# Performance work log

Measured on AMD Instinct MI355X. Metric: run time of the kernel, lower is better.

## Reference

```python
import jax, jax.numpy as jnp
import numpy as np

EPS = 1e-12  # torch F.normalize eps
K = 32       # num_clusters (hardcoded in module)

def l2norm(v, axis):
    n = jnp.sqrt(jnp.sum(v * v, axis=axis, keepdims=True))
    return v / jnp.maximum(n, EPS)

def setup_inputs() -> dict:
    key = jax.random.key(0)
    k1, k2, k3, k4 = jax.random.split(key, 4)
    B, M, D = 64, 128, 2048
    x = jax.random.normal(k1, (B, M, D), dtype=jnp.float32)
    # ragged lengths in [1, M]
    lengths = jax.random.randint(k2, (B,), 0, M, dtype=jnp.int32) + 1
    init_sc = 1.0 / np.sqrt(D)
    W = init_sc * jax.random.normal(k3, (K, D), dtype=jnp.float32)  # fc1.weight
    C = init_sc * jax.random.normal(k4, (K, D), dtype=jnp.float32)  # centroids
    return {"x": x, "lengths": lengths, "W": W, "C": C}

def reference(x, lengths, W, C):
    # x: [B,M,D] padded frames, lengths: [B] valid frame counts
    B, M, D = x.shape
    mask = (jnp.arange(M)[None, :] < lengths[:, None]).astype(x.dtype)  # [B,M]
    cnt = lengths.astype(x.dtype)[:, None]                              # [B,1]
    # avg pooling over valid (raw, un-normalized) frames
    avgpool = jnp.sum(x * mask[:, :, None], axis=1) / cnt               # [B,D]
    # per-frame L2 normalize
    xn = l2norm(x, axis=-1)                                             # [B,M,D]
    # soft assignment: linear (no bias) + softmax over clusters
    logits = jnp.einsum('bmd,kd->bmk', xn, W)
    a = jax.nn.softmax(logits, axis=-1) * mask[:, :, None]              # [B,M,K]
    # VLAD residual aggregation, GEMM form:
    # sum_m a[b,m,k]*(xn[b,m,:] - C[k,:]) = (a^T xn) - C * sum_m a
    ax = jnp.einsum('bmk,bmd->bkd', a, xn)                              # [B,K,D]
    asum = jnp.sum(a, axis=1)                                           # [B,K]
    vlad = ax - asum[:, :, None] * C[None, :, :]                        # [B,K,D]
    # intra-normalize per cluster, flatten, global L2 normalize
    vlad = l2norm(vlad, axis=2)
    vlad = vlad.reshape(B, K * D)
    vlad = l2norm(vlad, axis=1)
    return jnp.concatenate([avgpool, vlad], axis=1)                     # [B, D + K*D]
```

## Files before the change

kernel.cpp:

```cpp
#include <hip/hip_runtime.h>
#include <math.h>

#define BB 64
#define MM 128
#define DDIM 2048
#define KK 32
#define NFR (BB*MM)
#define OUTROW (DDIM + KK*DDIM)

typedef __attribute__((ext_vector_type(8))) short bf16x8;
typedef __attribute__((ext_vector_type(4))) float f32x4;

__device__ __forceinline__ short f2bf(float f) {
  unsigned u = __builtin_bit_cast(unsigned, f);
  u += 0x7fffu + ((u >> 16) & 1u);
  return (short)(u >> 16);
}
__device__ __forceinline__ unsigned pack2(float lo, float hi) {
  return (unsigned)(unsigned short)f2bf(lo) | ((unsigned)(unsigned short)f2bf(hi) << 16);
}

__global__ __launch_bounds__(256) void k_prep(const float* __restrict__ W,
                                              short* __restrict__ Wb) {
  int i = (blockIdx.x * 256 + threadIdx.x) * 8;
  float4 a = *(const float4*)(W + i);
  float4 b = *(const float4*)(W + i + 4);
  bf16x8 o = {f2bf(a.x), f2bf(a.y), f2bf(a.z), f2bf(a.w),
              f2bf(b.x), f2bf(b.y), f2bf(b.z), f2bf(b.w)};
  *(bf16x8*)(Wb + i) = o;
}

__global__ __launch_bounds__(256) void k_logits(const float* __restrict__ x,
    const int* __restrict__ lengths, const short* __restrict__ Wb,
    short* __restrict__ aT, float* __restrict__ asum_p) {
  const int t = threadIdx.x, wv = t >> 6, lane = t & 63;
  const int l15 = lane & 15, quad = lane >> 4;
  const int fg = blockIdx.x;
  const int g0 = fg * 16;
  const int b  = fg >> 3;
  const int m0 = (fg & 7) * 16;
  const int len = lengths[b];

  const float* xrow = x + (size_t)(g0 + l15) * DDIM + wv * 512 + quad * 8;
  const short* w0   = Wb + l15 * DDIM + wv * 512 + quad * 8;
  const short* w1   = w0 + 16 * DDIM;

  f32x4 c0 = {0.f, 0.f, 0.f, 0.f}, c1 = {0.f, 0.f, 0.f, 0.f};
  float ssq = 0.f;
  #pragma unroll
  for (int s = 0; s < 16; ++s) {
    float4 xa = *(const float4*)(xrow + s * 32);
    float4 xc = *(const float4*)(xrow + s * 32 + 4);
    ssq = fmaf(xa.x, xa.x, ssq); ssq = fmaf(xa.y, xa.y, ssq);
    ssq = fmaf(xa.z, xa.z, ssq); ssq = fmaf(xa.w, xa.w, ssq);
    ssq = fmaf(xc.x, xc.x, ssq); ssq = fmaf(xc.y, xc.y, ssq);
    ssq = fmaf(xc.z, xc.z, ssq); ssq = fmaf(xc.w, xc.w, ssq);
    bf16x8 A = {f2bf(xa.x), f2bf(xa.y), f2bf(xa.z), f2bf(xa.w),
                f2bf(xc.x), f2bf(xc.y), f2bf(xc.z), f2bf(xc.w)};
    bf16x8 B0 = *(const bf16x8*)(w0 + s * 32);
    bf16x8 B1 = *(const bf16x8*)(w1 + s * 32);
    c0 = __builtin_amdgcn_mfma_f32_16x16x32_bf16(A, B0, c0, 0, 0, 0);
    c1 = __builtin_amdgcn_mfma_f32_16x16x32_bf16(A, B1, c1, 0, 0, 0);
  }

  ssq += __shfl_xor(ssq, 16, 64);
  ssq += __shfl_xor(ssq, 32, 64);
  __shared__ float sq[4][16];
  __shared__ float lg[4][16][33];
  if (quad == 0) sq[wv][l15] = ssq;
  #pragma unroll
  for (int r = 0; r < 4; ++r) {
    lg[wv][quad * 4 + r][l15]      = c0[r];
    lg[wv][quad * 4 + r][16 + l15] = c1[r];
  }
  __syncthreads();

  const int fr = t >> 4, kk = (t & 15) * 2;
  float s0 = 0.f, s1 = 0.f;
  #pragma unroll
  for (int w = 0; w < 4; ++w) { s0 += lg[w][fr][kk]; s1 += lg[w][fr][kk + 1]; }
  float ss  = sq[0][fr] + sq[1][fr] + sq[2][fr] + sq[3][fr];
  float inv = 1.f / fmaxf(sqrtf(ss), 1e-12f);
  s0 *= inv; s1 *= inv;
  float mx = fmaxf(s0, s1);
  mx = fmaxf(mx, __shfl_xor(mx, 1, 64));
  mx = fmaxf(mx, __shfl_xor(mx, 2, 64));
  mx = fmaxf(mx, __shfl_xor(mx, 4, 64));
  mx = fmaxf(mx, __shfl_xor(mx, 8, 64));
  float e0 = __expf(s0 - mx), e1 = __expf(s1 - mx);
  float se = e0 + e1;
  se += __shfl_xor(se, 1, 64);
  se += __shfl_xor(se, 2, 64);
  se += __shfl_xor(se, 4, 64);
  se += __shfl_xor(se, 8, 64);
  const bool valid = (m0 + fr) < len;
  float rr = valid ? (1.f / se) : 0.f;
  float a0 = e0 * rr, a1 = e1 * rr;

  __syncthreads();
  lg[0][fr][kk] = a0; lg[0][fr][kk + 1] = a1;
  __syncthreads();
  if (t < KK) {
    float s = 0.f;
    #pragma unroll
    for (int f = 0; f < 16; ++f) s += lg[0][f][t];
    asum_p[(size_t)fg * KK + t] = s;
  }
  short* ap = aT + (size_t)b * KK * MM + m0 + fr;
  ap[(size_t)kk * MM]       = f2bf(a0 * inv);
  ap[(size_t)(kk + 1) * MM] = f2bf(a1 * inv);
}

__global__ __launch_bounds__(256) void k_vlad(const float* __restrict__ x,
    const int* __restrict__ lengths, const float* __restrict__ Cc,
    const short* __restrict__ aT, const float* __restrict__ asum_p,
    float* __restrict__ out, float* __restrict__ ssq_part) {
  const int t = threadIdx.x, wv = t >> 6, lane = t & 63;
  const int l15 = lane & 15, quad = lane >> 4;
  const int dc = blockIdx.x, b = blockIdx.y;
  const int dw0 = dc * 256 + wv * 64;
  const int len = lengths[b];

  __shared__ short xbt[4][64][40];
  __shared__ float asl[KK];
  __shared__ float ssw[4][33];

  if (t < KK) {
    float s = 0.f;
    #pragma unroll
    for (int p = 0; p < 8; ++p) s += asum_p[(size_t)(b * 8 + p) * KK + t];
    asl[t] = s;
  }

  const float* xb  = x  + (size_t)b * MM * DDIM;
  const short* at0 = aT + (size_t)b * KK * MM + l15 * MM + quad * 8;

  f32x4 acc[2][4];
  #pragma unroll
  for (int kt = 0; kt < 2; ++kt)
    #pragma unroll
    for (int nt = 0; nt < 4; ++nt) acc[kt][nt] = (f32x4){0.f, 0.f, 0.f, 0.f};
  float avg[4] = {0.f, 0.f, 0.f, 0.f};

  const int q4   = l15 * 4;
  const int mrow = (lane >> 4) * 2;

  for (int ms = 0; ms < 4; ++ms) {
    const int m0 = ms * 32;
    #pragma unroll
    for (int p = 0; p < 4; ++p) {
      int ml = p * 8 + mrow;
      int m  = m0 + ml;
      const float* xr = xb + (size_t)m * DDIM + dw0 + q4;
      float4 v0 = *(const float4*)xr;
      float4 v1 = *(const float4*)(xr + DDIM);
      float f0 = (m < len) ? 1.f : 0.f;
      float f1 = (m + 1 < len) ? 1.f : 0.f;
      avg[0] = fmaf(v0.x, f0, fmaf(v1.x, f1, avg[0]));
      avg[1] = fmaf(v0.y, f0, fmaf(v1.y, f1, avg[1]));
      avg[2] = fmaf(v0.z, f0, fmaf(v1.z, f1, avg[2]));
      avg[3] = fmaf(v0.w, f0, fmaf(v1.w, f1, avg[3]));
      *(unsigned*)&xbt[wv][q4 + 0][ml] = pack2(v0.x, v1.x);
      *(unsigned*)&xbt[wv][q4 + 1][ml] = pack2(v0.y, v1.y);
      *(unsigned*)&xbt[wv][q4 + 2][ml] = pack2(v0.z, v1.z);
      *(unsigned*)&xbt[wv][q4 + 3][ml] = pack2(v0.w, v1.w);
    }
    bf16x8 A0 = *(const bf16x8*)(at0 + m0);
    bf16x8 A1 = *(const bf16x8*)(at0 + 16 * MM + m0);
    #pragma unroll
    for (int nt = 0; nt < 4; ++nt) {
      bf16x8 B = *(const bf16x8*)&xbt[wv][nt * 16 + l15][quad * 8];
      acc[0][nt] = __builtin_amdgcn_mfma_f32_16x16x32_bf16(A0, B, acc[0][nt], 0, 0, 0);
      acc[1][nt] = __builtin_amdgcn_mfma_f32_16x16x32_bf16(A1, B, acc[1][nt], 0, 0, 0);
    }
  }

  #pragma unroll
  for (int c = 0; c < 4; ++c) {
    avg[c] += __shfl_xor(avg[c], 16, 64);
    avg[c] += __shfl_xor(avg[c], 32, 64);
  }
  if (quad == 0) {
    float rl = 1.f / (float)len;
    *(float4*)(out + (size_t)b * OUTROW + dw0 + q4) =
        make_float4(avg[0] * rl, avg[1] * rl, avg[2] * rl, avg[3] * rl);
  }

  __syncthreads();
  float* orow = out + (size_t)b * OUTROW + DDIM;
  #pragma unroll
  for (int kt = 0; kt < 2; ++kt) {
    #pragma unroll
    for (int r = 0; r < 4; ++r) {
      const int k = kt * 16 + quad * 4 + r;
      const float as = asl[k];
      float sqv = 0.f;
      #pragma unroll
      for (int nt = 0; nt < 4; ++nt) {
        const int d = dw0 + nt * 16 + l15;
        float v = acc[kt][nt][r] - as * Cc[(size_t)k * DDIM + d];
        orow[(size_t)k * DDIM + d] = v;
        sqv = fmaf(v, v, sqv);
      }
      sqv += __shfl_xor(sqv, 1, 64);
      sqv += __shfl_xor(sqv, 2, 64);
      sqv += __shfl_xor(sqv, 4, 64);
      sqv += __shfl_xor(sqv, 8, 64);
      if (l15 == 0) ssw[wv][k] = sqv;
    }
  }
  __syncthreads();
  if (t < KK)
    ssq_part[((size_t)dc * BB + b) * KK + t] =
        ssw[0][t] + ssw[1][t] + ssw[2][t] + ssw[3][t];
}

__global__ __launch_bounds__(256) void k_norm(const float* __restrict__ ssq_part,
    float* __restrict__ out) {
  const int t = threadIdx.x;
  const int k = blockIdx.x;
  const int b = blockIdx.y;
  __shared__ float ssk[32];
  if (t < 32) {
    float sk = 0.f;
    #pragma unroll
    for (int dc = 0; dc < 8; ++dc)
      sk += ssq_part[((size_t)dc * BB + b) * KK + t];
    ssk[t] = sk;
  }
  __syncthreads();
  float gss = 0.f, iv_own = 0.f;
  #pragma unroll
  for (int kk = 0; kk < 32; ++kk) {
    float nk = sqrtf(ssk[kk]);
    float iv = 1.f / fmaxf(nk, 1e-12f);
    float nn = nk * iv;
    gss += nn * nn;
    if (kk == k) iv_own = iv;
  }
  float sc = iv_own / fmaxf(sqrtf(gss), 1e-12f);
  float* row = out + (size_t)b * OUTROW + DDIM + (size_t)k * DDIM;
  #pragma unroll
  for (int h = 0; h < 2; ++h) {
    float4* p = (float4*)(row + h * 1024 + t * 4);
    float4 v = *p;
    v.x *= sc; v.y *= sc; v.z *= sc; v.w *= sc;
    *p = v;
  }
}

extern "C" void kernel_launch(void* const* d_in, const int* in_sizes, int n_in,
                              void* d_out, int out_size, void* d_ws, size_t ws_size,
                              hipStream_t stream) {
  const float* x       = (const float*)d_in[0];
  const int*   lengths = (const int*)d_in[1];
  const float* W       = (const float*)d_in[2];
  const float* C       = (const float*)d_in[3];
  float* out = (float*)d_out;

  short* Wb     = (short*)d_ws;
  short* aT     = Wb + (size_t)KK * DDIM;
  float* asum_p = (float*)(aT + (size_t)BB * KK * MM);
  float* ssqp   = asum_p + (size_t)512 * KK;

  k_prep  <<<dim3(32),     256, 0, stream>>>(W, Wb);
  k_logits<<<dim3(512),    256, 0, stream>>>(x, lengths, Wb, aT, asum_p);
  k_vlad  <<<dim3(8, BB),  256, 0, stream>>>(x, lengths, C, aT, asum_p, out, ssqp);
  k_norm  <<<dim3(KK, BB), 256, 0, stream>>>(ssqp, out);
}
```

Before: 146.1 us.

## Fuse four kernels into one cooperative kernel with grid-wide syncs

```diff
diff --git a/kernel.cpp b/kernel.cpp
--- a/kernel.cpp
+++ b/kernel.cpp
@@ -1,5 +1,8 @@
 #include <hip/hip_runtime.h>
+#include <hip/hip_cooperative_groups.h>
 #include <math.h>
+
+namespace cg = cooperative_groups;
 
 #define BB 64
 #define MM 128
@@ -20,232 +23,234 @@
   return (unsigned)(unsigned short)f2bf(lo) | ((unsigned)(unsigned short)f2bf(hi) << 16);
 }
 
-__global__ __launch_bounds__(256) void k_prep(const float* __restrict__ W,
-                                              short* __restrict__ Wb) {
-  int i = (blockIdx.x * 256 + threadIdx.x) * 8;
-  float4 a = *(const float4*)(W + i);
-  float4 b = *(const float4*)(W + i + 4);
-  bf16x8 o = {f2bf(a.x), f2bf(a.y), f2bf(a.z), f2bf(a.w),
-              f2bf(b.x), f2bf(b.y), f2bf(b.z), f2bf(b.w)};
-  *(bf16x8*)(Wb + i) = o;
-}
-
-__global__ __launch_bounds__(256) void k_logits(const float* __restrict__ x,
-    const int* __restrict__ lengths, const short* __restrict__ Wb,
-    short* __restrict__ aT, float* __restrict__ asum_p) {
+__global__ __launch_bounds__(256, 2) void k_fused(
+    const float* __restrict__ x, const int* __restrict__ lengths,
+    const float* __restrict__ W, const float* __restrict__ Cc,
+    float* __restrict__ out, short* __restrict__ Wb,
+    short* __restrict__ aT, float* __restrict__ asum_p,
+    float* __restrict__ ssqp) {
+  cg::grid_group grid = cg::this_grid();
   const int t = threadIdx.x, wv = t >> 6, lane = t & 63;
   const int l15 = lane & 15, quad = lane >> 4;
-  const int fg = blockIdx.x;
-  const int g0 = fg * 16;
-  const int b  = fg >> 3;
-  const int m0 = (fg & 7) * 16;
-  const int len = lengths[b];
-
-  const float* xrow = x + (size_t)(g0 + l15) * DDIM + wv * 512 + quad * 8;
-  const short* w0   = Wb + l15 * DDIM + wv * 512 + quad * 8;
-  const short* w1   = w0 + 16 * DDIM;
-
-  f32x4 c0 = {0.f, 0.f, 0.f, 0.f}, c1 = {0.f, 0.f, 0.f, 0.f};
-  float ssq = 0.f;
-  #pragma unroll
-  for (int s = 0; s < 16; ++s) {
-    float4 xa = *(const float4*)(xrow + s * 32);
-    float4 xc = *(const float4*)(xrow + s * 32 + 4);
-    ssq = fmaf(xa.x, xa.x, ssq); ssq = fmaf(xa.y, xa.y, ssq);
-    ssq = fmaf(xa.z, xa.z, ssq); ssq = fmaf(xa.w, xa.w, ssq);
-    ssq = fmaf(xc.x, xc.x, ssq); ssq = fmaf(xc.y, xc.y, ssq);
-    ssq = fmaf(xc.z, xc.z, ssq); ssq = fmaf(xc.w, xc.w, ssq);
-    bf16x8 A = {f2bf(xa.x), f2bf(xa.y), f2bf(xa.z), f2bf(xa.w),
-                f2bf(xc.x), f2bf(xc.y), f2bf(xc.z), f2bf(xc.w)};
-    bf16x8 B0 = *(const bf16x8*)(w0 + s * 32);
-    bf16x8 B1 = *(const bf16x8*)(w1 + s * 32);
-    c0 = __builtin_amdgcn_mfma_f32_16x16x32_bf16(A, B0, c0, 0, 0, 0);
-    c1 = __builtin_amdgcn_mfma_f32_16x16x32_bf16(A, B1, c1, 0, 0, 0);
-  }
-
-  ssq += __shfl_xor(ssq, 16, 64);
-  ssq += __shfl_xor(ssq, 32, 64);
+  const int blk = blockIdx.x;
+
   __shared__ float sq[4][16];
   __shared__ float lg[4][16][33];
-  if (quad == 0) sq[wv][l15] = ssq;
-  #pragma unroll
-  for (int r = 0; r < 4; ++r) {
-    lg[wv][quad * 4 + r][l15]      = c0[r];
-    lg[wv][quad * 4 + r][16 + l15] = c1[r];
-  }
-  __syncthreads();
-
-  const int fr = t >> 4, kk = (t & 15) * 2;
-  float s0 = 0.f, s1 = 0.f;
-  #pragma unroll
-  for (int w = 0; w < 4; ++w) { s0 += lg[w][fr][kk]; s1 += lg[w][fr][kk + 1]; }
-  float ss  = sq[0][fr] + sq[1][fr] + sq[2][fr] + sq[3][fr];
-  float inv = 1.f / fmaxf(sqrtf(ss), 1e-12f);
-  s0 *= inv; s1 *= inv;
-  float mx = fmaxf(s0, s1);
-  mx = fmaxf(mx, __shfl_xor(mx, 1, 64));
-  mx = fmaxf(mx, __shfl_xor(mx, 2, 64));
-  mx = fmaxf(mx, __shfl_xor(mx, 4, 64));
-  mx = fmaxf(mx, __shfl_xor(mx, 8, 64));
-  float e0 = __expf(s0 - mx), e1 = __expf(s1 - mx);
-  float se = e0 + e1;
-  se += __shfl_xor(se, 1, 64);
-  se += __shfl_xor(se, 2, 64);
-  se += __shfl_xor(se, 4, 64);
-  se += __shfl_xor(se, 8, 64);
-  const bool valid = (m0 + fr) < len;
-  float rr = valid ? (1.f / se) : 0.f;
-  float a0 = e0 * rr, a1 = e1 * rr;
-
-  __syncthreads();
-  lg[0][fr][kk] = a0; lg[0][fr][kk + 1] = a1;
-  __syncthreads();
-  if (t < KK) {
-    float s = 0.f;
-    #pragma unroll
-    for (int f = 0; f < 16; ++f) s += lg[0][f][t];
-    asum_p[(size_t)fg * KK + t] = s;
-  }
-  short* ap = aT + (size_t)b * KK * MM + m0 + fr;
-  ap[(size_t)kk * MM]       = f2bf(a0 * inv);
-  ap[(size_t)(kk + 1) * MM] = f2bf(a1 * inv);
-}
-
-__global__ __launch_bounds__(256) void k_vlad(const float* __restrict__ x,
-    const int* __restrict__ lengths, const float* __restrict__ Cc,
-    const short* __restrict__ aT, const float* __restrict__ asum_p,
-    float* __restrict__ out, float* __restrict__ ssq_part) {
-  const int t = threadIdx.x, wv = t >> 6, lane = t & 63;
-  const int l15 = lane & 15, quad = lane >> 4;
-  const int dc = blockIdx.x, b = blockIdx.y;
-  const int dw0 = dc * 256 + wv * 64;
-  const int len = lengths[b];
-
   __shared__ short xbt[4][64][40];
   __shared__ float asl[KK];
   __shared__ float ssw[4][33];
-
-  if (t < KK) {
-    float s = 0.f;
-    #pragma unroll
-    for (int p = 0; p < 8; ++p) s += asum_p[(size_t)(b * 8 + p) * KK + t];
-    asl[t] = s;
-  }
-
-  const float* xb  = x  + (size_t)b * MM * DDIM;
-  const short* at0 = aT + (size_t)b * KK * MM + l15 * MM + quad * 8;
-
-  f32x4 acc[2][4];
-  #pragma unroll
-  for (int kt = 0; kt < 2; ++kt)
-    #pragma unroll
-    for (int nt = 0; nt < 4; ++nt) acc[kt][nt] = (f32x4){0.f, 0.f, 0.f, 0.f};
-  float avg[4] = {0.f, 0.f, 0.f, 0.f};
-
-  const int q4   = l15 * 4;
-  const int mrow = (lane >> 4) * 2;
-
-  for (int ms = 0; ms < 4; ++ms) {
-    const int m0 = ms * 32;
-    #pragma unroll
-    for (int p = 0; p < 4; ++p) {
-      int ml = p * 8 + mrow;
-      int m  = m0 + ml;
-      const float* xr = xb + (size_t)m * DDIM + dw0 + q4;
-      float4 v0 = *(const float4*)xr;
-      float4 v1 = *(const float4*)(xr + DDIM);
-      float f0 = (m < len) ? 1.f : 0.f;
-      float f1 = (m + 1 < len) ? 1.f : 0.f;
-      avg[0] = fmaf(v0.x, f0, fmaf(v1.x, f1, avg[0]));
-      avg[1] = fmaf(v0.y, f0, fmaf(v1.y, f1, avg[1]));
-      avg[2] = fmaf(v0.z, f0, fmaf(v1.z, f1, avg[2]));
-      avg[3] = fmaf(v0.w, f0, fmaf(v1.w, f1, avg[3]));
-      *(unsigned*)&xbt[wv][q4 + 0][ml] = pack2(v0.x, v1.x);
-      *(unsigned*)&xbt[wv][q4 + 1][ml] = pack2(v0.y, v1.y);
-      *(unsigned*)&xbt[wv][q4 + 2][ml] = pack2(v0.z, v1.z);
-      *(unsigned*)&xbt[wv][q4 + 3][ml] = pack2(v0.w, v1.w);
-    }
-    bf16x8 A0 = *(const bf16x8*)(at0 + m0);
-    bf16x8 A1 = *(const bf16x8*)(at0 + 16 * MM + m0);
-    #pragma unroll
-    for (int nt = 0; nt < 4; ++nt) {
-      bf16x8 B = *(const bf16x8*)&xbt[wv][nt * 16 + l15][quad * 8];
-      acc[0][nt] = __builtin_amdgcn_mfma_f32_16x16x32_bf16(A0, B, acc[0][nt], 0, 0, 0);
-      acc[1][nt] = __builtin_amdgcn_mfma_f32_16x16x32_bf16(A1, B, acc[1][nt], 0, 0, 0);
-    }
-  }
-
-  #pragma unroll
-  for (int c = 0; c < 4; ++c) {
-    avg[c] += __shfl_xor(avg[c], 16, 64);
-    avg[c] += __shfl_xor(avg[c], 32, 64);
-  }
-  if (quad == 0) {
-    float rl = 1.f / (float)len;
-    *(float4*)(out + (size_t)b * OUTROW + dw0 + q4) =
-        make_float4(avg[0] * rl, avg[1] * rl, avg[2] * rl, avg[3] * rl);
-  }
-
-  __syncthreads();
-  float* orow = out + (size_t)b * OUTROW + DDIM;
-  #pragma unroll
-  for (int kt = 0; kt < 2; ++kt) {
+  __shared__ float ssk[KK];
+
+  if (blk < 32) {
+    int i = (blk * 256 + t) * 8;
+    float4 a = *(const float4*)(W + i);
+    float4 b = *(const float4*)(W + i + 4);
+    bf16x8 o = {f2bf(a.x), f2bf(a.y), f2bf(a.z), f2bf(a.w),
+                f2bf(b.x), f2bf(b.y), f2bf(b.z), f2bf(b.w)};
+    *(bf16x8*)(Wb + i) = o;
+  }
+  grid.sync();
+
+  {
+    const int fg = blk;
+    const int g0 = fg * 16;
+    const int b  = fg >> 3;
+    const int m0 = (fg & 7) * 16;
+    const int len = lengths[b];
+
+    const float* xrow = x + (size_t)(g0 + l15) * DDIM + wv * 512 + quad * 8;
+    const short* w0   = Wb + l15 * DDIM + wv * 512 + quad * 8;
+    const short* w1   = w0 + 16 * DDIM;
+
+    f32x4 c0 = {0.f, 0.f, 0.f, 0.f}, c1 = {0.f, 0.f, 0.f, 0.f};
+    float ssq = 0.f;
+    #pragma unroll
+    for (int s = 0; s < 16; ++s) {
+      float4 xa = *(const float4*)(xrow + s * 32);
+      float4 xc = *(const float4*)(xrow + s * 32 + 4);
+      ssq = fmaf(xa.x, xa.x, ssq); ssq = fmaf(xa.y, xa.y, ssq);
+      ssq = fmaf(xa.z, xa.z, ssq); ssq = fmaf(xa.w, xa.w, ssq);
+      ssq = fmaf(xc.x, xc.x, ssq); ssq = fmaf(xc.y, xc.y, ssq);
+      ssq = fmaf(xc.z, xc.z, ssq); ssq = fmaf(xc.w, xc.w, ssq);
+      bf16x8 A = {f2bf(xa.x), f2bf(xa.y), f2bf(xa.z), f2bf(xa.w),
+                  f2bf(xc.x), f2bf(xc.y), f2bf(xc.z), f2bf(xc.w)};
+      bf16x8 B0 = *(const bf16x8*)(w0 + s * 32);
+      bf16x8 B1 = *(const bf16x8*)(w1 + s * 32);
+      c0 = __builtin_amdgcn_mfma_f32_16x16x32_bf16(A, B0, c0, 0, 0, 0);
+      c1 = __builtin_amdgcn_mfma_f32_16x16x32_bf16(A, B1, c1, 0, 0, 0);
+    }
+
+    ssq += __shfl_xor(ssq, 16, 64);
+    ssq += __shfl_xor(ssq, 32, 64);
+    if (quad == 0) sq[wv][l15] = ssq;
     #pragma unroll
     for (int r = 0; r < 4; ++r) {
-      const int k = kt * 16 + quad * 4 + r;
-      const float as = asl[k];
-      float sqv = 0.f;
+      lg[wv][quad * 4 + r][l15]      = c0[r];
+      lg[wv][quad * 4 + r][16 + l15] = c1[r];
+    }
+    __syncthreads();
+
+    const int fr = t >> 4, kk = (t & 15) * 2;
+    float s0 = 0.f, s1 = 0.f;
+    #pragma unroll
+    for (int w = 0; w < 4; ++w) { s0 += lg[w][fr][kk]; s1 += lg[w][fr][kk + 1]; }
+    float ss  = sq[0][fr] + sq[1][fr] + sq[2][fr] + sq[3][fr];
+    float inv = 1.f / fmaxf(sqrtf(ss), 1e-12f);
+    s0 *= inv; s1 *= inv;
+    float mx = fmaxf(s0, s1);
+    mx = fmaxf(mx, __shfl_xor(mx, 1, 64));
+    mx = fmaxf(mx, __shfl_xor(mx, 2, 64));
+    mx = fmaxf(mx, __shfl_xor(mx, 4, 64));
+    mx = fmaxf(mx, __shfl_xor(mx, 8, 64));
+    float e0 = __expf(s0 - mx), e1 = __expf(s1 - mx);
+    float se = e0 + e1;
+    se += __shfl_xor(se, 1, 64);
+    se += __shfl_xor(se, 2, 64);
+    se += __shfl_xor(se, 4, 64);
+    se += __shfl_xor(se, 8, 64);
+    const bool valid = (m0 + fr) < len;
+    float rr = valid ? (1.f / se) : 0.f;
+    float a0 = e0 * rr, a1 = e1 * rr;
+
+    __syncthreads();
+    lg[0][fr][kk] = a0; lg[0][fr][kk + 1] = a1;
+    __syncthreads();
+    if (t < KK) {
+      float s = 0.f;
+      #pragma unroll
+      for (int f = 0; f < 16; ++f) s += lg[0][f][t];
+      asum_p[(size_t)fg * KK + t] = s;
+    }
+    short* ap = aT + (size_t)b * KK * MM + m0 + fr;
+    ap[(size_t)kk * MM]       = f2bf(a0 * inv);
+    ap[(size_t)(kk + 1) * MM] = f2bf(a1 * inv);
+  }
+  grid.sync();
+
+  {
+    const int dc = blk & 7, b = blk >> 3;
+    const int dw0 = dc * 256 + wv * 64;
+    const int len = lengths[b];
+
+    if (t < KK) {
+      float s = 0.f;
+      #pragma unroll
+      for (int p = 0; p < 8; ++p) s += asum_p[(size_t)(b * 8 + p) * KK + t];
+      asl[t] = s;
+    }
+
+    const float* xb  = x  + (size_t)b * MM * DDIM;
+    const short* at0 = aT + (size_t)b * KK * MM + l15 * MM + quad * 8;
+
+    f32x4 acc[2][4];
+    #pragma unroll
+    for (int kt = 0; kt < 2; ++kt)
+      #pragma unroll
+      for (int nt = 0; nt < 4; ++nt) acc[kt][nt] = (f32x4){0.f, 0.f, 0.f, 0.f};
+    float avg[4] = {0.f, 0.f, 0.f, 0.f};
+
+    const int q4   = l15 * 4;
+    const int mrow = quad * 2;
+    const int keyw = l15 & 3;
+    const int keyr = (l15 >> 2) & 3;
+
+    for (int ms = 0; ms < 4; ++ms) {
+      const int m0 = ms * 32;
+      #pragma unroll
+      for (int p = 0; p < 4; ++p) {
+        int ml = p * 8 + mrow;
+        int m  = m0 + ml;
+        const float* xr = xb + (size_t)m * DDIM + dw0 + q4;
+        float4 v0 = *(const float4*)xr;
+        float4 v1 = *(const float4*)(xr + DDIM);
+        float f0 = (m < len) ? 1.f : 0.f;
+        float f1 = (m + 1 < len) ? 1.f : 0.f;
+        avg[0] = fmaf(v0.x, f0, fmaf(v1.x, f1, avg[0]));
+        avg[1] = fmaf(v0.y, f0, fmaf(v1.y, f1, avg[1]));
+        avg[2] = fmaf(v0.z, f0, fmaf(v1.z, f1, avg[2]));
+        avg[3] = fmaf(v0.w, f0, fmaf(v1.w, f1, avg[3]));
+        int mls = (p ^ keyw) * 8 + mrow;
+        *(unsigned*)&xbt[wv][q4 + 0][mls] = pack2(v0.x, v1.x);
+        *(unsigned*)&xbt[wv][q4 + 1][mls] = pack2(v0.y, v1.y);
+        *(unsigned*)&xbt[wv][q4 + 2][mls] = pack2(v0.z, v1.z);
+        *(unsigned*)&xbt[wv][q4 + 3][mls] = pack2(v0.w, v1.w);
+      }
+      bf16x8 A0 = *(const bf16x8*)(at0 + m0);
+      bf16x8 A1 = *(const bf16x8*)(at0 + 16 * MM + m0);
       #pragma unroll
       for (int nt = 0; nt < 4; ++nt) {
-        const int d = dw0 + nt * 16 + l15;
-        float v = acc[kt][nt][r] - as * Cc[(size_t)k * DDIM + d];
-        orow[(size_t)k * DDIM + d] = v;
-        sqv = fmaf(v, v, sqv);
+        bf16x8 B = *(const bf16x8*)&xbt[wv][nt * 16 + l15][(quad ^ keyr) * 8];
+        acc[0][nt] = __builtin_amdgcn_mfma_f32_16x16x32_bf16(A0, B, acc[0][nt], 0, 0, 0);
+        acc[1][nt] = __builtin_amdgcn_mfma_f32_16x16x32_bf16(A1, B, acc[1][nt], 0, 0, 0);
       }
-      sqv += __shfl_xor(sqv, 1, 64);
-      sqv += __shfl_xor(sqv, 2, 64);
-      sqv += __shfl_xor(sqv, 4, 64);
-      sqv += __shfl_xor(sqv, 8, 64);
-      if (l15 == 0) ssw[wv][k] = sqv;
-    }
-  }
-  __syncthreads();
-  if (t < KK)
-    ssq_part[((size_t)dc * BB + b) * KK + t] =
-        ssw[0][t] + ssw[1][t] + ssw[2][t] + ssw[3][t];
-}
-
-__global__ __launch_bounds__(256) void k_norm(const float* __restrict__ ssq_part,
-    float* __restrict__ out) {
-  const int t = threadIdx.x;
-  const int k = blockIdx.x;
-  const int b = blockIdx.y;
-  __shared__ float ssk[32];
-  if (t < 32) {
-    float sk = 0.f;
-    #pragma unroll
-    for (int dc = 0; dc < 8; ++dc)
-      sk += ssq_part[((size_t)dc * BB + b) * KK + t];
-    ssk[t] = sk;
-  }
-  __syncthreads();
-  float gss = 0.f, iv_own = 0.f;
-  #pragma unroll
-  for (int kk = 0; kk < 32; ++kk) {
-    float nk = sqrtf(ssk[kk]);
-    float iv = 1.f / fmaxf(nk, 1e-12f);
-    float nn = nk * iv;
-    gss += nn * nn;
-    if (kk == k) iv_own = iv;
-  }
-  float sc = iv_own / fmaxf(sqrtf(gss), 1e-12f);
-  float* row = out + (size_t)b * OUTROW + DDIM + (size_t)k * DDIM;
-  #pragma unroll
-  for (int h = 0; h < 2; ++h) {
-    float4* p = (float4*)(row + h * 1024 + t * 4);
-    float4 v = *p;
-    v.x *= sc; v.y *= sc; v.z *= sc; v.w *= sc;
-    *p = v;
+    }
+
+    #pragma unroll
+    for (int c = 0; c < 4; ++c) {
+      avg[c] += __shfl_xor(avg[c], 16, 64);
+      avg[c] += __shfl_xor(avg[c], 32, 64);
+    }
+    if (quad == 0) {
+      float rl = 1.f / (float)len;
+      *(float4*)(out + (size_t)b * OUTROW + dw0 + q4) =
+          make_float4(avg[0] * rl, avg[1] * rl, avg[2] * rl, avg[3] * rl);
+    }
+
+    __syncthreads();
+    float* orow = out + (size_t)b * OUTROW + DDIM;
+    #pragma unroll
+    for (int kt = 0; kt < 2; ++kt) {
+      #pragma unroll
+      for (int r = 0; r < 4; ++r) {
+        const int k = kt * 16 + quad * 4 + r;
+        const float as = asl[k];
+        float sqv = 0.f;
+        #pragma unroll
+        for (int nt = 0; nt < 4; ++nt) {
+          const int d = dw0 + nt * 16 + l15;
+          float v = acc[kt][nt][r] - as * Cc[(size_t)k * DDIM + d];
+          orow[(size_t)k * DDIM + d] = v;
+          sqv = fmaf(v, v, sqv);
+        }
+        sqv += __shfl_xor(sqv, 1, 64);
+        sqv += __shfl_xor(sqv, 2, 64);
+        sqv += __shfl_xor(sqv, 4, 64);
+        sqv += __shfl_xor(sqv, 8, 64);
+        if (l15 == 0) ssw[wv][k] = sqv;
+      }
+    }
+    __syncthreads();
+    if (t < KK)
+      ssqp[((size_t)dc * BB + b) * KK + t] =
+          ssw[0][t] + ssw[1][t] + ssw[2][t] + ssw[3][t];
+  }
+  grid.sync();
+
+  {
+    const int dc = blk & 7, b = blk >> 3;
+    if (t < KK) {
+      float sk = 0.f;
+      #pragma unroll
+      for (int p = 0; p < 8; ++p)
+        sk += ssqp[((size_t)p * BB + b) * KK + t];
+      ssk[t] = sk;
+    }
+    __syncthreads();
+    float gss = 0.f;
+    #pragma unroll
+    for (int k = 0; k < KK; ++k) {
+      float nk = sqrtf(ssk[k]);
+      float nn = nk * (1.f / fmaxf(nk, 1e-12f));
+      gss += nn * nn;
+    }
+    float ginv = 1.f / fmaxf(sqrtf(gss), 1e-12f);
+    float* orow = out + (size_t)b * OUTROW + DDIM + dc * 256 + t;
+    #pragma unroll
+    for (int k = 0; k < KK; ++k) {
+      float iv = 1.f / fmaxf(sqrtf(ssk[k]), 1e-12f);
+      float v = orow[(size_t)k * DDIM];
+      orow[(size_t)k * DDIM] = v * (iv * ginv);
+    }
   }
 }
 
@@ -263,8 +268,9 @@
   float* asum_p = (float*)(aT + (size_t)BB * KK * MM);
   float* ssqp   = asum_p + (size_t)512 * KK;
 
-  k_prep  <<<dim3(32),     256, 0, stream>>>(W, Wb);
-  k_logits<<<dim3(512),    256, 0, stream>>>(x, lengths, Wb, aT, asum_p);
-  k_vlad  <<<dim3(8, BB),  256, 0, stream>>>(x, lengths, C, aT, asum_p, out, ssqp);
-  k_norm  <<<dim3(KK, BB), 256, 0, stream>>>(ssqp, out);
-}
+  void* args[] = {(void*)&x, (void*)&lengths, (void*)&W, (void*)&C,
+                  (void*)&out, (void*)&Wb, (void*)&aT, (void*)&asum_p,
+                  (void*)&ssqp};
+  hipLaunchCooperativeKernel((const void*)k_fused, dim3(512), dim3(256),
+                             args, 0, stream);
+}
```

After: 293.9 us. 2.01x slower.

## Batch global loads up front, skip padded-frame loads, swizzle LDS transpose

Applied to the files above, without the earlier changes.

```diff
diff --git a/kernel.cpp b/kernel.cpp
--- a/kernel.cpp
+++ b/kernel.cpp
@@ -30,7 +30,7 @@
   *(bf16x8*)(Wb + i) = o;
 }
 
-__global__ __launch_bounds__(256) void k_logits(const float* __restrict__ x,
+__global__ __launch_bounds__(256, 2) void k_logits(const float* __restrict__ x,
     const int* __restrict__ lengths, const short* __restrict__ Wb,
     short* __restrict__ aT, float* __restrict__ asum_p) {
   const int t = threadIdx.x, wv = t >> 6, lane = t & 63;
@@ -40,6 +40,7 @@
   const int b  = fg >> 3;
   const int m0 = (fg & 7) * 16;
   const int len = lengths[b];
+  const bool av = (m0 + l15) < len;
 
   const float* xrow = x + (size_t)(g0 + l15) * DDIM + wv * 512 + quad * 8;
   const short* w0   = Wb + l15 * DDIM + wv * 512 + quad * 8;
@@ -48,19 +49,33 @@
   f32x4 c0 = {0.f, 0.f, 0.f, 0.f}, c1 = {0.f, 0.f, 0.f, 0.f};
   float ssq = 0.f;
   #pragma unroll
-  for (int s = 0; s < 16; ++s) {
-    float4 xa = *(const float4*)(xrow + s * 32);
-    float4 xc = *(const float4*)(xrow + s * 32 + 4);
-    ssq = fmaf(xa.x, xa.x, ssq); ssq = fmaf(xa.y, xa.y, ssq);
-    ssq = fmaf(xa.z, xa.z, ssq); ssq = fmaf(xa.w, xa.w, ssq);
-    ssq = fmaf(xc.x, xc.x, ssq); ssq = fmaf(xc.y, xc.y, ssq);
-    ssq = fmaf(xc.z, xc.z, ssq); ssq = fmaf(xc.w, xc.w, ssq);
-    bf16x8 A = {f2bf(xa.x), f2bf(xa.y), f2bf(xa.z), f2bf(xa.w),
-                f2bf(xc.x), f2bf(xc.y), f2bf(xc.z), f2bf(xc.w)};
-    bf16x8 B0 = *(const bf16x8*)(w0 + s * 32);
-    bf16x8 B1 = *(const bf16x8*)(w1 + s * 32);
-    c0 = __builtin_amdgcn_mfma_f32_16x16x32_bf16(A, B0, c0, 0, 0, 0);
-    c1 = __builtin_amdgcn_mfma_f32_16x16x32_bf16(A, B1, c1, 0, 0, 0);
+  for (int h = 0; h < 2; ++h) {
+    float4 xa[8], xc[8];
+    bf16x8 B0[8], B1[8];
+    #pragma unroll
+    for (int s = 0; s < 8; ++s) {
+      const int so = h * 8 + s;
+      if (av) {
+        xa[s] = *(const float4*)(xrow + so * 32);
+        xc[s] = *(const float4*)(xrow + so * 32 + 4);
+      } else {
+        xa[s] = make_float4(0.f, 0.f, 0.f, 0.f);
+        xc[s] = make_float4(0.f, 0.f, 0.f, 0.f);
+      }
+      B0[s] = *(const bf16x8*)(w0 + so * 32);
+      B1[s] = *(const bf16x8*)(w1 + so * 32);
+    }
+    #pragma unroll
+    for (int s = 0; s < 8; ++s) {
+      ssq = fmaf(xa[s].x, xa[s].x, ssq); ssq = fmaf(xa[s].y, xa[s].y, ssq);
+      ssq = fmaf(xa[s].z, xa[s].z, ssq); ssq = fmaf(xa[s].w, xa[s].w, ssq);
+      ssq = fmaf(xc[s].x, xc[s].x, ssq); ssq = fmaf(xc[s].y, xc[s].y, ssq);
+      ssq = fmaf(xc[s].z, xc[s].z, ssq); ssq = fmaf(xc[s].w, xc[s].w, ssq);
+      bf16x8 A = {f2bf(xa[s].x), f2bf(xa[s].y), f2bf(xa[s].z), f2bf(xa[s].w),
+                  f2bf(xc[s].x), f2bf(xc[s].y), f2bf(xc[s].z), f2bf(xc[s].w)};
+      c0 = __builtin_amdgcn_mfma_f32_16x16x32_bf16(A, B0[s], c0, 0, 0, 0);
+      c1 = __builtin_amdgcn_mfma_f32_16x16x32_bf16(A, B1[s], c1, 0, 0, 0);
+    }
   }
 
   ssq += __shfl_xor(ssq, 16, 64);
@@ -111,7 +126,7 @@
   ap[(size_t)(kk + 1) * MM] = f2bf(a1 * inv);
 }
 
-__global__ __launch_bounds__(256) void k_vlad(const float* __restrict__ x,
+__global__ __launch_bounds__(256, 2) void k_vlad(const float* __restrict__ x,
     const int* __restrict__ lengths, const float* __restrict__ Cc,
     const short* __restrict__ aT, const float* __restrict__ asum_p,
     float* __restrict__ out, float* __restrict__ ssq_part) {
@@ -135,43 +150,63 @@
   const float* xb  = x  + (size_t)b * MM * DDIM;
   const short* at0 = aT + (size_t)b * KK * MM + l15 * MM + quad * 8;
 
+  const int q4   = l15 * 4;
+  const int mrow = quad * 2;
+  const int keyw = l15 & 3;
+  const int keyr = (l15 >> 2) & 3;
+
+  bf16x8 A0[4], A1[4];
+  #pragma unroll
+  for (int ms = 0; ms < 4; ++ms) {
+    A0[ms] = *(const bf16x8*)(at0 + ms * 32);
+    A1[ms] = *(const bf16x8*)(at0 + 16 * MM + ms * 32);
+  }
+
+  float4 v0[16], v1[16];
+  #pragma unroll
+  for (int ms = 0; ms < 4; ++ms) {
+    #pragma unroll
+    for (int p = 0; p < 4; ++p) {
+      const int m = ms * 32 + p * 8 + mrow;
+      const float* xr = xb + (size_t)m * DDIM + dw0 + q4;
+      v0[ms * 4 + p] = (m < len) ? *(const float4*)xr
+                                 : make_float4(0.f, 0.f, 0.f, 0.f);
+      v1[ms * 4 + p] = (m + 1 < len) ? *(const float4*)(xr + DDIM)
+                                     : make_float4(0.f, 0.f, 0.f, 0.f);
+    }
+  }
+
+  float avg[4] = {0.f, 0.f, 0.f, 0.f};
+  #pragma unroll
+  for (int i = 0; i < 16; ++i) {
+    avg[0] += v0[i].x + v1[i].x;
+    avg[1] += v0[i].y + v1[i].y;
+    avg[2] += v0[i].z + v1[i].z;
+    avg[3] += v0[i].w + v1[i].w;
+  }
+
   f32x4 acc[2][4];
   #pragma unroll
   for (int kt = 0; kt < 2; ++kt)
     #pragma unroll
     for (int nt = 0; nt < 4; ++nt) acc[kt][nt] = (f32x4){0.f, 0.f, 0.f, 0.f};
-  float avg[4] = {0.f, 0.f, 0.f, 0.f};
-
-  const int q4   = l15 * 4;
-  const int mrow = (lane >> 4) * 2;
-
+
+  #pragma unroll
   for (int ms = 0; ms < 4; ++ms) {
-    const int m0 = ms * 32;
     #pragma unroll
     for (int p = 0; p < 4; ++p) {
-      int ml = p * 8 + mrow;
-      int m  = m0 + ml;
-      const float* xr = xb + (size_t)m * DDIM + dw0 + q4;
-      float4 v0 = *(const float4*)xr;
-      float4 v1 = *(const float4*)(xr + DDIM);
-      float f0 = (m < len) ? 1.f : 0.f;
-      float f1 = (m + 1 < len) ? 1.f : 0.f;
-      avg[0] = fmaf(v0.x, f0, fmaf(v1.x, f1, avg[0]));
-      avg[1] = fmaf(v0.y, f0, fmaf(v1.y, f1, avg[1]));
-      avg[2] = fmaf(v0.z, f0, fmaf(v1.z, f1, avg[2]));
-      avg[3] = fmaf(v0.w, f0, fmaf(v1.w, f1, avg[3]));
-      *(unsigned*)&xbt[wv][q4 + 0][ml] = pack2(v0.x, v1.x);
-      *(unsigned*)&xbt[wv][q4 + 1][ml] = pack2(v0.y, v1.y);
-      *(unsigned*)&xbt[wv][q4 + 2][ml] = pack2(v0.z, v1.z);
-      *(unsigned*)&xbt[wv][q4 + 3][ml] = pack2(v0.w, v1.w);
-    }
-    bf16x8 A0 = *(const bf16x8*)(at0 + m0);
-    bf16x8 A1 = *(const bf16x8*)(at0 + 16 * MM + m0);
+      const int i = ms * 4 + p;
+      const int mls = (p ^ keyw) * 8 + mrow;
+      *(unsigned*)&xbt[wv][q4 + 0][mls] = pack2(v0[i].x, v1[i].x);
+      *(unsigned*)&xbt[wv][q4 + 1][mls] = pack2(v0[i].y, v1[i].y);
+      *(unsigned*)&xbt[wv][q4 + 2][mls] = pack2(v0[i].z, v1[i].z);
+      *(unsigned*)&xbt[wv][q4 + 3][mls] = pack2(v0[i].w, v1[i].w);
+    }
     #pragma unroll
     for (int nt = 0; nt < 4; ++nt) {
-      bf16x8 B = *(const bf16x8*)&xbt[wv][nt * 16 + l15][quad * 8];
-      acc[0][nt] = __builtin_amdgcn_mfma_f32_16x16x32_bf16(A0, B, acc[0][nt], 0, 0, 0);
-      acc[1][nt] = __builtin_amdgcn_mfma_f32_16x16x32_bf16(A1, B, acc[1][nt], 0, 0, 0);
+      bf16x8 B = *(const bf16x8*)&xbt[wv][nt * 16 + l15][(quad ^ keyr) * 8];
+      acc[0][nt] = __builtin_amdgcn_mfma_f32_16x16x32_bf16(A0[ms], B, acc[0][nt], 0, 0, 0);
+      acc[1][nt] = __builtin_amdgcn_mfma_f32_16x16x32_bf16(A1[ms], B, acc[1][nt], 0, 0, 0);
     }
   }
 
```

New measurement: 145.9 us. About the same (-0.1%).
